# Optimization experiments

Measured on AMD Instinct MI355X. Metric: run time of the kernel, lower is better.

Reference implementation:

```python
import jax, jax.numpy as jnp
import numpy as np

N = 50000   # nodes
E = 600000  # edges
F = 128     # num_features (= in_channels = out_channels of EvolveGCNO)
C = 2       # num_classes


def setup_inputs() -> dict:
    key = jax.random.key(0)
    ks = jax.random.split(key, 8)
    s = 1.0 / np.sqrt(F)
    x = jax.random.normal(ks[0], (N, F), jnp.float32)
    edge_index = jax.random.randint(ks[1], (2, E), 0, N, jnp.int64)
    W0 = jax.random.uniform(ks[2], (F, F), jnp.float32, -s, s)      # initial GCN weight (glorot-ish)
    w_ih = jax.random.uniform(ks[3], (4 * F, F), jnp.float32, -s, s)  # LSTM input-hidden
    w_hh = jax.random.uniform(ks[4], (4 * F, F), jnp.float32, -s, s)  # LSTM hidden-hidden
    b_ih = jax.random.uniform(ks[5], (4 * F,), jnp.float32, -s, s)
    b_hh = jax.random.uniform(ks[6], (4 * F,), jnp.float32, -s, s)
    gcn_bias = jnp.zeros((F,), jnp.float32)
    Wc = jax.random.uniform(ks[7], (C, F), jnp.float32, -s, s)       # classifier nn.Linear(F, C)
    bc = jnp.zeros((C,), jnp.float32)
    return dict(x=x, W0=W0, w_ih=w_ih, w_hh=w_hh, b_ih=b_ih, b_hh=b_hh,
                gcn_bias=gcn_bias, Wc=Wc, bc=bc, edge_index=edge_index)


def reference(x, W0, w_ih, w_hh, b_ih, b_hh, gcn_bias, Wc, bc, edge_index):
    n = x.shape[0]
    # --- EvolveGCN-O weight evolution: one LSTM step on the FxF weight,
    # rows of W0 are the LSTM "batch", initial hidden/cell state are zero.
    gates = W0 @ w_ih.T + b_ih + b_hh            # [F, 4F]  (h=0 so w_hh term vanishes)
    i, f, g, o = jnp.split(gates, 4, axis=1)     # PyTorch gate order: i, f, g, o
    c = jax.nn.sigmoid(i) * jnp.tanh(g)          # c0 = 0 -> f-gate term drops
    W = jax.nn.sigmoid(o) * jnp.tanh(c)          # evolved GCN weight [F, F]

    # --- GCN normalization with self-loops: D^-1/2 (A + I) D^-1/2
    loop = jnp.arange(n, dtype=edge_index.dtype)
    row = jnp.concatenate([edge_index[0], loop])  # source
    col = jnp.concatenate([edge_index[1], loop])  # target
    ew = jnp.ones(row.shape[0], x.dtype)
    deg = jax.ops.segment_sum(ew, col, num_segments=n)
    dis = jnp.where(deg > 0, jax.lax.rsqrt(jnp.maximum(deg, 1.0)), 0.0)
    norm = dis[row] * dis[col]                    # [E+N]

    # --- GCNConv_Fixed_W: transform then aggregate messages at targets
    xw = x @ W                                    # [N, F]
    msg = norm[:, None] * xw[row]                 # gather + scale
    h = jax.ops.segment_sum(msg, col, num_segments=n) + gcn_bias  # scatter-add

    h = jax.nn.relu(h)
    # dropout(p=0.3) is identity in eval mode
    return h @ Wc.T + bc                          # [N, C]
```

## Files before the change

kernel.cpp:

```cpp
#include <hip/hip_runtime.h>
#include <hip/hip_bf16.h>

#define F 128
#define CAP 32

typedef __bf16 bf16x8 __attribute__((ext_vector_type(8)));
typedef float f32x4 __attribute__((ext_vector_type(4)));

static __device__ __forceinline__ unsigned int f2bfbits(float f) {
  unsigned int u = __float_as_uint(f);
  return (u + 0x7fffu + ((u >> 16) & 1u)) >> 16;
}

__global__ __launch_bounds__(256) void lstm_fill_kernel(
    const float* __restrict__ W0, const float* __restrict__ w_ih,
    const float* __restrict__ b_ih, const float* __restrict__ b_hh,
    unsigned short* __restrict__ Wt, const int* __restrict__ row,
    const int* __restrict__ col, int* __restrict__ deg,
    unsigned short* __restrict__ bucket, int* __restrict__ ovf_cnt,
    int* __restrict__ ovf, int e) {
  __shared__ __align__(16) float srow[4][F];
  __shared__ float sg[4][4 * F];
  int b = blockIdx.x, t = threadIdx.x;
  if (b < 32) {
    int r0 = b * 4;
    for (int i = t; i < 4 * F; i += 256)
      srow[i >> 7][i & 127] = W0[(size_t)(r0 + (i >> 7)) * F + (i & 127)];
    __syncthreads();
#pragma unroll
    for (int half = 0; half < 2; half++) {
      int gc = t + half * 256;
      float acc[4] = {0.f, 0.f, 0.f, 0.f};
      const float4* wv4 = (const float4*)(w_ih + (size_t)gc * F);
#pragma unroll 4
      for (int k4 = 0; k4 < F / 4; k4++) {
        float4 w = wv4[k4];
#pragma unroll
        for (int i = 0; i < 4; i++) {
          float4 s = *(const float4*)&srow[i][k4 * 4];
          acc[i] = fmaf(s.x, w.x, fmaf(s.y, w.y, fmaf(s.z, w.z, fmaf(s.w, w.w, acc[i]))));
        }
      }
      float bias = b_ih[gc] + b_hh[gc];
#pragma unroll
      for (int i = 0; i < 4; i++) sg[i][gc] = acc[i] + bias;
    }
    __syncthreads();
#pragma unroll
    for (int half = 0; half < 2; half++) {
      int idx2 = t + half * 256;
      int rr = idx2 >> 7, c = idx2 & 127;
      float gi = sg[rr][c], gg = sg[rr][c + 2 * F], go = sg[rr][c + 3 * F];
      float si = 1.f / (1.f + expf(-gi));
      float so = 1.f / (1.f + expf(-go));
      float cc2 = si * tanhf(gg);
      Wt[(size_t)c * F + r0 + rr] = (unsigned short)f2bfbits(so * tanhf(cc2));
    }
  } else {
    int stride = ((int)gridDim.x - 32) * 256;
    for (int i = (b - 32) * 256 + t; i < e; i += stride) {
      int c = col[i];
      int r = row[i];
      int p = atomicAdd(&deg[c], 1);
      if (p < CAP) {
        bucket[(size_t)c * CAP + p] = (unsigned short)r;
      } else {
        int q = atomicAdd(ovf_cnt, 1);
        ovf[2 * q + 0] = c;
        ovf[2 * q + 1] = r;
      }
    }
  }
}

__global__ __launch_bounds__(256) void xw_dis_kernel(
    const float* __restrict__ x, const unsigned short* __restrict__ Wt,
    unsigned short* __restrict__ xwb, const int* __restrict__ deg,
    float* __restrict__ dis, int n, int NT) {
  int b = blockIdx.x, t = threadIdx.x;
  if (b < NT) {
    int w = t >> 6, l = t & 63;
    int q = l >> 4, m = l & 15;
    int m0 = b * 64 + w * 16;
    int arow = m0 + m;
    bf16x8 a[4];
    const float4* xr4 = (const float4*)(x + (size_t)arow * F);
    bool rv = arow < n;
#pragma unroll
    for (int kc = 0; kc < 4; kc++) {
      uint4 pk = make_uint4(0u, 0u, 0u, 0u);
      if (rv) {
        float4 v0 = xr4[kc * 8 + q * 2 + 0];
        float4 v1 = xr4[kc * 8 + q * 2 + 1];
        pk.x = f2bfbits(v0.x) | (f2bfbits(v0.y) << 16);
        pk.y = f2bfbits(v0.z) | (f2bfbits(v0.w) << 16);
        pk.z = f2bfbits(v1.x) | (f2bfbits(v1.y) << 16);
        pk.w = f2bfbits(v1.z) | (f2bfbits(v1.w) << 16);
      }
      a[kc] = __builtin_bit_cast(bf16x8, pk);
    }
#pragma unroll
    for (int nc = 0; nc < 8; nc++) {
      f32x4 acc = {0.f, 0.f, 0.f, 0.f};
#pragma unroll
      for (int kc = 0; kc < 4; kc++) {
        uint4 bu = *(const uint4*)(Wt + (size_t)(nc * 16 + m) * F + kc * 32 + q * 8);
        acc = __builtin_amdgcn_mfma_f32_16x16x32_bf16(
            a[kc], __builtin_bit_cast(bf16x8, bu), acc, 0, 0, 0);
      }
#pragma unroll
      for (int r = 0; r < 4; r++) {
        int gr = m0 + q * 4 + r;
        if (gr < n)
          xwb[(size_t)gr * F + nc * 16 + m] = (unsigned short)f2bfbits(acc[r]);
      }
    }
  } else {
    int stride = ((int)gridDim.x - NT) * 256;
    for (int i = (b - NT) * 256 + t; i < n; i += stride)
      dis[i] = rsqrtf((float)(deg[i] + 1));
  }
}

__global__ __launch_bounds__(256) void agg_kernel(
    const int* __restrict__ deg, const unsigned short* __restrict__ bucket,
    const float* __restrict__ dis, const unsigned int* __restrict__ xwb,
    const int* __restrict__ ovf_cnt, const int* __restrict__ ovf,
    const float* __restrict__ gcn_bias, const float* __restrict__ Wc,
    const float* __restrict__ bc, float* __restrict__ out, int n) {
  int wave = threadIdx.x >> 6;
  int lane = threadIdx.x & 63;
  int v = blockIdx.x * 4 + wave;
  if (v >= n) return;
  float dv = dis[v];
  float ax, ay;
  {
    unsigned int u = xwb[(size_t)v * 64 + lane];
    float sl = dv * dv;
    ax = sl * __uint_as_float(u << 16);
    ay = sl * __uint_as_float(u & 0xffff0000u);
  }
  int d = deg[v];
  int eend = d < CAP ? d : CAP;
  const unsigned short* bkt = bucket + (size_t)v * CAP;
  int j = 0;
  for (; j + 8 <= eend; j += 8) {
    int s[8];
    float nr[8];
    unsigned int u[8];
#pragma unroll
    for (int q = 0; q < 8; q++) s[q] = bkt[j + q];
#pragma unroll
    for (int q = 0; q < 8; q++) nr[q] = dis[s[q]] * dv;
#pragma unroll
    for (int q = 0; q < 8; q++) u[q] = xwb[(size_t)s[q] * 64 + lane];
#pragma unroll
    for (int q = 0; q < 8; q++) {
      ax = fmaf(nr[q], __uint_as_float(u[q] << 16), ax);
      ay = fmaf(nr[q], __uint_as_float(u[q] & 0xffff0000u), ay);
    }
  }
  for (; j < eend; j++) {
    int s = bkt[j];
    float nr = dis[s] * dv;
    unsigned int u = xwb[(size_t)s * 64 + lane];
    ax = fmaf(nr, __uint_as_float(u << 16), ax);
    ay = fmaf(nr, __uint_as_float(u & 0xffff0000u), ay);
  }
  if (d > CAP) {
    int oc = *ovf_cnt;
    for (int k = 0; k < oc; k++) {
      if (ovf[2 * k] == v) {
        int s = ovf[2 * k + 1];
        float nr = dis[s] * dv;
        unsigned int u = xwb[(size_t)s * 64 + lane];
        ax = fmaf(nr, __uint_as_float(u << 16), ax);
        ay = fmaf(nr, __uint_as_float(u & 0xffff0000u), ay);
      }
    }
  }
  int f0 = lane * 2;
  float h0 = fmaxf(ax + gcn_bias[f0], 0.f);
  float h1 = fmaxf(ay + gcn_bias[f0 + 1], 0.f);
  float a0 = h0 * Wc[f0] + h1 * Wc[f0 + 1];
  float a1 = h0 * Wc[F + f0] + h1 * Wc[F + f0 + 1];
#pragma unroll
  for (int off = 32; off > 0; off >>= 1) {
    a0 += __shfl_down(a0, off);
    a1 += __shfl_down(a1, off);
  }
  if (lane == 0) {
    out[(size_t)v * 2 + 0] = a0 + bc[0];
    out[(size_t)v * 2 + 1] = a1 + bc[1];
  }
}

extern "C" void kernel_launch(void* const* d_in, const int* in_sizes, int n_in,
                              void* d_out, int out_size, void* d_ws, size_t ws_size,
                              hipStream_t stream) {
  const float* x        = (const float*)d_in[0];
  const float* W0       = (const float*)d_in[1];
  const float* w_ih     = (const float*)d_in[2];
  const float* b_ih     = (const float*)d_in[4];
  const float* b_hh     = (const float*)d_in[5];
  const float* gcn_bias = (const float*)d_in[6];
  const float* Wc       = (const float*)d_in[7];
  const float* bc       = (const float*)d_in[8];
  const int*   ei       = (const int*)d_in[9];

  const int n = in_sizes[0] / F;
  const int e = in_sizes[9] / 2;
  const int* row = ei;
  const int* col = ei + e;

  char* wsb = (char*)d_ws;
  unsigned short* Wt = (unsigned short*)wsb;  wsb += 32768;
  size_t n4 = ((size_t)n * 4 + 255) & ~(size_t)255;
  int*   deg     = (int*)wsb;                 wsb += n4;
  int*   ovf_cnt = deg + n;
  float* dis     = (float*)wsb;               wsb += n4;
  int*   ovf     = (int*)wsb;                 wsb += 8192;
  unsigned short* bucket = (unsigned short*)wsb;
  wsb += (size_t)n * CAP * 2;
  unsigned short* xwb = (unsigned short*)wsb;

  const int NT = (n + 63) / 64;

  hipMemsetAsync(deg, 0, n4, stream);

  lstm_fill_kernel<<<32 + 1500, 256, 0, stream>>>(W0, w_ih, b_ih, b_hh, Wt,
                                                  row, col, deg, bucket,
                                                  ovf_cnt, ovf, e);

  xw_dis_kernel<<<NT + 64, 256, 0, stream>>>(x, Wt, xwb, deg, dis, n, NT);

  agg_kernel<<<(n + 3) / 4, 256, 0, stream>>>(deg, bucket, dis,
                                              (const unsigned int*)xwb,
                                              ovf_cnt, ovf, gcn_bias, Wc, bc,
                                              (float*)d_out, n);
}
```

Baseline: 182.7 us.

## Overlap bucket fill with xW GEMM and compute norms on the fly

Removes the memset by zeroing deg inside the LSTM kernel. Moves the edge-bucket fill into the same launch as the xW MFMA GEMM so the two can run concurrently. The fill is split into 8 column-residue groups, so each block re-reads all edges but only handles one eighth, which aims to reduce atomic contention. The dis array is dropped and rsqrt(deg+1) is computed inline in aggregation, trading a stored array for extra recomputation plus 8x redundant reads of the edge columns.

Result: faster. 166.7 us (-8.8%).

```diff
diff --git a/kernel.cpp b/kernel.cpp
--- a/kernel.cpp
+++ b/kernel.cpp
@@ -3,6 +3,7 @@
 
 #define F 128
 #define CAP 32
+#define NF 1024
 
 typedef __bf16 bf16x8 __attribute__((ext_vector_type(8)));
 typedef float f32x4 __attribute__((ext_vector_type(4)));
@@ -12,13 +13,11 @@
   return (u + 0x7fffu + ((u >> 16) & 1u)) >> 16;
 }
 
-__global__ __launch_bounds__(256) void lstm_fill_kernel(
+__global__ __launch_bounds__(256) void lstm_zero_kernel(
     const float* __restrict__ W0, const float* __restrict__ w_ih,
     const float* __restrict__ b_ih, const float* __restrict__ b_hh,
-    unsigned short* __restrict__ Wt, const int* __restrict__ row,
-    const int* __restrict__ col, int* __restrict__ deg,
-    unsigned short* __restrict__ bucket, int* __restrict__ ovf_cnt,
-    int* __restrict__ ovf, int e) {
+    unsigned short* __restrict__ Wt, int* __restrict__ deg,
+    int* __restrict__ ovf_cnt, int n) {
   __shared__ __align__(16) float srow[4][F];
   __shared__ float sg[4][4 * F];
   int b = blockIdx.x, t = threadIdx.x;
@@ -58,30 +57,40 @@
     }
   } else {
     int stride = ((int)gridDim.x - 32) * 256;
-    for (int i = (b - 32) * 256 + t; i < e; i += stride) {
+    for (int i = (b - 32) * 256 + t; i < n; i += stride) deg[i] = 0;
+    if (b == 32 && t == 0) *ovf_cnt = 0;
+  }
+}
+
+__global__ __launch_bounds__(256) void fill_xw_kernel(
+    const int* __restrict__ row, const int* __restrict__ col,
+    int* __restrict__ deg, unsigned short* __restrict__ bucket,
+    int* __restrict__ ovf_cnt, int* __restrict__ ovf,
+    const float* __restrict__ x, const unsigned short* __restrict__ Wt,
+    unsigned short* __restrict__ xwb, int n, int e) {
+  int b = blockIdx.x, t = threadIdx.x;
+  if (b < NF) {
+    int g = b & 7;
+    int cg = b >> 3;
+    const int stride = (NF / 8) * 256;
+    for (int i = cg * 256 + t; i < e; i += stride) {
       int c = col[i];
-      int r = row[i];
-      int p = atomicAdd(&deg[c], 1);
-      if (p < CAP) {
-        bucket[(size_t)c * CAP + p] = (unsigned short)r;
-      } else {
-        int q = atomicAdd(ovf_cnt, 1);
-        ovf[2 * q + 0] = c;
-        ovf[2 * q + 1] = r;
-      }
-    }
-  }
-}
-
-__global__ __launch_bounds__(256) void xw_dis_kernel(
-    const float* __restrict__ x, const unsigned short* __restrict__ Wt,
-    unsigned short* __restrict__ xwb, const int* __restrict__ deg,
-    float* __restrict__ dis, int n, int NT) {
-  int b = blockIdx.x, t = threadIdx.x;
-  if (b < NT) {
+      if ((c & 7) == g) {
+        int r = row[i];
+        int p = atomicAdd(&deg[c], 1);
+        if (p < CAP) {
+          bucket[(size_t)c * CAP + p] = (unsigned short)r;
+        } else {
+          int q = atomicAdd(ovf_cnt, 1);
+          ovf[2 * q + 0] = c;
+          ovf[2 * q + 1] = r;
+        }
+      }
+    }
+  } else {
     int w = t >> 6, l = t & 63;
     int q = l >> 4, m = l & 15;
-    int m0 = b * 64 + w * 16;
+    int m0 = (b - NF) * 64 + w * 16;
     int arow = m0 + m;
     bf16x8 a[4];
     const float4* xr4 = (const float4*)(x + (size_t)arow * F);
@@ -115,24 +124,21 @@
           xwb[(size_t)gr * F + nc * 16 + m] = (unsigned short)f2bfbits(acc[r]);
       }
     }
-  } else {
-    int stride = ((int)gridDim.x - NT) * 256;
-    for (int i = (b - NT) * 256 + t; i < n; i += stride)
-      dis[i] = rsqrtf((float)(deg[i] + 1));
   }
 }
 
 __global__ __launch_bounds__(256) void agg_kernel(
     const int* __restrict__ deg, const unsigned short* __restrict__ bucket,
-    const float* __restrict__ dis, const unsigned int* __restrict__ xwb,
-    const int* __restrict__ ovf_cnt, const int* __restrict__ ovf,
-    const float* __restrict__ gcn_bias, const float* __restrict__ Wc,
-    const float* __restrict__ bc, float* __restrict__ out, int n) {
+    const unsigned int* __restrict__ xwb, const int* __restrict__ ovf_cnt,
+    const int* __restrict__ ovf, const float* __restrict__ gcn_bias,
+    const float* __restrict__ Wc, const float* __restrict__ bc,
+    float* __restrict__ out, int n) {
   int wave = threadIdx.x >> 6;
   int lane = threadIdx.x & 63;
   int v = blockIdx.x * 4 + wave;
   if (v >= n) return;
-  float dv = dis[v];
+  int d = deg[v];
+  float dv = rsqrtf((float)(d + 1));
   float ax, ay;
   {
     unsigned int u = xwb[(size_t)v * 64 + lane];
@@ -140,7 +146,6 @@
     ax = sl * __uint_as_float(u << 16);
     ay = sl * __uint_as_float(u & 0xffff0000u);
   }
-  int d = deg[v];
   int eend = d < CAP ? d : CAP;
   const unsigned short* bkt = bucket + (size_t)v * CAP;
   int j = 0;
@@ -151,7 +156,7 @@
 #pragma unroll
     for (int q = 0; q < 8; q++) s[q] = bkt[j + q];
 #pragma unroll
-    for (int q = 0; q < 8; q++) nr[q] = dis[s[q]] * dv;
+    for (int q = 0; q < 8; q++) nr[q] = rsqrtf((float)(deg[s[q]] + 1)) * dv;
 #pragma unroll
     for (int q = 0; q < 8; q++) u[q] = xwb[(size_t)s[q] * 64 + lane];
 #pragma unroll
@@ -162,7 +167,7 @@
   }
   for (; j < eend; j++) {
     int s = bkt[j];
-    float nr = dis[s] * dv;
+    float nr = rsqrtf((float)(deg[s] + 1)) * dv;
     unsigned int u = xwb[(size_t)s * 64 + lane];
     ax = fmaf(nr, __uint_as_float(u << 16), ax);
     ay = fmaf(nr, __uint_as_float(u & 0xffff0000u), ay);
@@ -172,7 +177,7 @@
     for (int k = 0; k < oc; k++) {
       if (ovf[2 * k] == v) {
         int s = ovf[2 * k + 1];
-        float nr = dis[s] * dv;
+        float nr = rsqrtf((float)(deg[s] + 1)) * dv;
         unsigned int u = xwb[(size_t)s * 64 + lane];
         ax = fmaf(nr, __uint_as_float(u << 16), ax);
         ay = fmaf(nr, __uint_as_float(u & 0xffff0000u), ay);
@@ -218,7 +223,6 @@
   size_t n4 = ((size_t)n * 4 + 255) & ~(size_t)255;
   int*   deg     = (int*)wsb;                 wsb += n4;
   int*   ovf_cnt = deg + n;
-  float* dis     = (float*)wsb;               wsb += n4;
   int*   ovf     = (int*)wsb;                 wsb += 8192;
   unsigned short* bucket = (unsigned short*)wsb;
   wsb += (size_t)n * CAP * 2;
@@ -226,15 +230,13 @@
 
   const int NT = (n + 63) / 64;
 
-  hipMemsetAsync(deg, 0, n4, stream);
-
-  lstm_fill_kernel<<<32 + 1500, 256, 0, stream>>>(W0, w_ih, b_ih, b_hh, Wt,
-                                                  row, col, deg, bucket,
-                                                  ovf_cnt, ovf, e);
-
-  xw_dis_kernel<<<NT + 64, 256, 0, stream>>>(x, Wt, xwb, deg, dis, n, NT);
-
-  agg_kernel<<<(n + 3) / 4, 256, 0, stream>>>(deg, bucket, dis,
+  lstm_zero_kernel<<<32 + 128, 256, 0, stream>>>(W0, w_ih, b_ih, b_hh, Wt,
+                                                 deg, ovf_cnt, n);
+
+  fill_xw_kernel<<<NF + NT, 256, 0, stream>>>(row, col, deg, bucket, ovf_cnt,
+                                              ovf, x, Wt, xwb, n, e);
+
+  agg_kernel<<<(n + 3) / 4, 256, 0, stream>>>(deg, bucket,
                                               (const unsigned int*)xwb,
                                               ovf_cnt, ovf, gcn_bias, Wc, bc,
                                               (float*)d_out, n);
```
